# Kernel optimization log

Hardware: AMD Instinct MI355X
Metric: run time of the kernel (lower is better)

Reference implementation:

```python
import jax, jax.numpy as jnp
import numpy as np

BETA, ALPHA, NS_STEPS = 0.9, 1.0, 1
D_MODEL, D_STATE, D_CONV, EXPAND = 768, 16, 4, 2
D_INNER = EXPAND * D_MODEL
DT_RANK = -(-D_MODEL // 16)  # ceil(d_model/16) = 48
B, L = 2, 1024


def setup_inputs() -> dict:
    key = jax.random.key(0)
    ks = jax.random.split(key, 8)
    s = lambda k, shape, sc=0.02: jax.random.normal(k, shape, jnp.float32) * sc
    return {
        "hidden_states": jax.random.normal(ks[0], (B, L, D_MODEL), jnp.float32),
        "in_proj_w": s(ks[1], (2 * D_INNER, D_MODEL)),
        "conv_w": s(ks[2], (D_INNER, 1, D_CONV), 0.2),
        "conv_b": jnp.zeros((D_INNER,), jnp.float32),
        "x_proj_w": s(ks[3], (DT_RANK + 2 * D_STATE, D_INNER)),
        "dt_head_w": s(ks[4], (D_INNER, DT_RANK)),
        "dt_head_b": s(ks[5], (D_INNER,), 0.1),
        "out_proj_w": s(ks[6], (D_MODEL, D_INNER)),
        "D": jnp.ones((D_INNER,), jnp.float32),
    }


def _newton_schulz(G, steps):
    """Muon-style quintic Newton-Schulz orthogonalization of (b, d, n) with d >= n."""
    a, b, c = 3.4445, -4.7750, 2.0315
    X = G / (jnp.linalg.norm(G, axis=(-2, -1), keepdims=True) + 1e-7)
    X = X.swapaxes(-2, -1)  # (b, n, d): rows <= cols
    for _ in range(steps):
        A = X @ X.swapaxes(-2, -1)       # (b, n, n) small Gram
        Bm = b * A + c * (A @ A)
        X = a * X + Bm @ X
    return X.swapaxes(-2, -1)            # back to (b, d, n)


def reference(hidden_states, in_proj_w, conv_w, conv_b, x_proj_w, dt_head_w, dt_head_b, out_proj_w, D):
    Bz, Lz, _ = hidden_states.shape
    dtype = hidden_states.dtype
    # input projection -> x, z  (B, L, d_inner) each
    xz = jnp.einsum('bld,ed->ble', hidden_states, in_proj_w)
    x, z = jnp.split(xz, 2, axis=-1)
    # causal depthwise conv over time + SiLU
    xc = jax.lax.conv_general_dilated(
        x.swapaxes(1, 2), conv_w, (1,), [(D_CONV - 1, 0)],
        dimension_numbers=('NCH', 'OIH', 'NCH'), feature_group_count=D_INNER)
    x = jax.nn.silu(xc.swapaxes(1, 2) + conv_b)  # (B, L, d_inner)
    # projections for dt / k / q
    x_dbl = jnp.einsum('bld,ed->ble', x, x_proj_w)
    dt_low, k, q = jnp.split(x_dbl, [DT_RANK, DT_RANK + D_STATE], axis=-1)
    dt = jnp.einsum('blr,dr->bld', dt_low, dt_head_w)  # (B, L, d_inner), bias applied in scan

    def step(carry, inp):
        v, h = carry  # velocity / hidden states, each (b, d_inner, d_state)
        x_t, dt_t, k_t, q_t = inp
        dt_t = jax.nn.sigmoid(dt_t + dt_head_b)                              # (b, d)
        dt_t = dt_t / (1.0 + dt_t * jnp.sum(k_t * k_t, axis=-1, keepdims=True))
        dA = 1.0 - dt_t[:, :, None] * (k_t * k_t)[:, None, :]                # (b, d, n)
        G = (dt_t * x_t)[:, :, None] * k_t[:, None, :]                       # dt * u * k
        v = BETA * v + ALPHA * _newton_schulz(G, NS_STEPS)
        h = dA * h + v
        y_t = jnp.einsum('bdn,bn->bd', h, q_t) + D * x_t
        return (v, h), y_t

    init = (jnp.zeros((Bz, D_INNER, D_STATE), dtype),
            jnp.zeros((Bz, D_INNER, D_STATE), dtype))
    xs = (x.swapaxes(0, 1), dt.swapaxes(0, 1), k.swapaxes(0, 1), q.swapaxes(0, 1))
    _, y = jax.lax.scan(step, init, xs)        # (L, B, d_inner)
    y = y.swapaxes(0, 1) * jax.nn.silu(z)      # gate
    return jnp.einsum('bld,od->blo', y, out_proj_w)
```

## Files before the change

### kernel.cpp

```cpp
#include <hip/hip_runtime.h>

#define D_MODEL 768
#define D_STATE 16
#define D_INNER 1536
#define DT_RANK 48
#define NB 2
#define LSEQ 1024
#define NROWS (NB * LSEQ)
#define CCH 16
#define CLEN (LSEQ / CCH)
#define STP 16
#define BETA_CL 1.1790185e-03f
#define OUT_ELEMS (NROWS * D_MODEL)

typedef __attribute__((ext_vector_type(4))) float f32x4;
typedef __attribute__((ext_vector_type(8))) short s16x8;
typedef __attribute__((ext_vector_type(8))) unsigned short u16x8;
typedef __attribute__((ext_vector_type(4))) unsigned short u16x4;

__device__ __forceinline__ unsigned short f2bu(float f) {
  unsigned int x = __builtin_bit_cast(unsigned int, f);
  x += 0x7fffu + ((x >> 16) & 1u);
  return (unsigned short)(x >> 16);
}

typedef __attribute__((address_space(3))) unsigned int as3u32;
typedef __attribute__((address_space(1))) const unsigned int as1u32;
__device__ __forceinline__ void gload16(const unsigned short* g, unsigned short* l) {
  __builtin_amdgcn_global_load_lds((as1u32*)g, (as3u32*)l, 16, 0, 0);
}

#define CVT_TOTAL 663552
#define Z1_GROUPS 20480
__global__ __launch_bounds__(256) void cvt5z_kernel(const float* __restrict__ s0,
                                                    const float* __restrict__ s1,
                                                    const float* __restrict__ s2,
                                                    const float* __restrict__ s3,
                                                    const float* __restrict__ s4,
                                                    unsigned short* __restrict__ d0,
                                                    unsigned short* __restrict__ d1,
                                                    unsigned short* __restrict__ d2,
                                                    unsigned short* __restrict__ d3,
                                                    unsigned short* __restrict__ d4,
                                                    float* __restrict__ z1) {
  int g = blockIdx.x * 256 + threadIdx.x;
  if (g >= CVT_TOTAL) {
    int zg = g - CVT_TOTAL;
    f32x4 zero = {0.f, 0.f, 0.f, 0.f};
    if (zg < Z1_GROUPS) {
      *(f32x4*)(z1 + zg * 8) = zero;
      *(f32x4*)(z1 + zg * 8 + 4) = zero;
    }
    return;
  }
  const float* s;
  unsigned short* d;
  int base;
  if (g < 196608)      { s = s0; d = d0; base = 0; }
  else if (g < 491520) { s = s1; d = d1; base = 196608; }
  else if (g < 506880) { s = s2; d = d2; base = 491520; }
  else if (g < 516096) { s = s3; d = d3; base = 506880; }
  else                 { s = s4; d = d4; base = 516096; }
  int i = (g - base) * 8;
  f32x4 a = *(const f32x4*)(s + i);
  f32x4 b = *(const f32x4*)(s + i + 4);
  u16x8 o;
#pragma unroll
  for (int j = 0; j < 4; j++) { o[j] = f2bu(a[j]); o[4 + j] = f2bu(b[j]); }
  *(u16x8*)(d + i) = o;
}

template <bool PARTIAL>
__global__ __launch_bounds__(256) void gemm128(const unsigned short* __restrict__ A,
                                               const unsigned short* __restrict__ B,
                                               float* __restrict__ C, int K,
                                               int lda, int ldb, int ldc, int kseg_len) {
  __shared__ __align__(16) unsigned short As[2][128 * 32];
  __shared__ __align__(16) unsigned short Bs[2][128 * 32];
  const int m0 = blockIdx.y * 128, n0 = blockIdx.x * 128;
  const int kbeg = blockIdx.z * kseg_len;
  const int kend = kbeg + kseg_len;
  const int t = threadIdx.x;
  const int wave = t >> 6, lane = t & 63;
  const int wm = wave >> 1, wn = wave & 1;
  const int quad = lane >> 4, l16 = lane & 15;
  const int srow = lane >> 2;
  const int kcol = (lane & 3) * 8;

  float* Cp = C;
  if constexpr (PARTIAL) Cp = C + (size_t)blockIdx.z * (size_t)gridDim.y * 128 * ldc;

  auto stage = [&](int bi, int k0) {
#pragma unroll
    for (int r = 0; r < 2; r++) {
      const int seg = r * 64 + wave * 16;
      gload16(A + (size_t)(m0 + seg + srow) * lda + k0 + kcol, &As[bi][seg * 32]);
      gload16(B + (size_t)(n0 + seg + srow) * ldb + k0 + kcol, &Bs[bi][seg * 32]);
    }
  };

  f32x4 acc[4][4] = {};
  stage(0, kbeg);
  __syncthreads();
  int buf = 0;
  for (int k0 = kbeg; k0 < kend; k0 += 32) {
    if (k0 + 32 < kend) stage(buf ^ 1, k0 + 32);
    s16x8 af[4], bf[4];
#pragma unroll
    for (int i = 0; i < 4; i++) {
      af[i] = *(const s16x8*)&As[buf][(wm * 64 + i * 16 + l16) * 32 + quad * 8];
      bf[i] = *(const s16x8*)&Bs[buf][(wn * 64 + i * 16 + l16) * 32 + quad * 8];
    }
#pragma unroll
    for (int mi = 0; mi < 4; mi++)
#pragma unroll
      for (int ni = 0; ni < 4; ni++)
        acc[mi][ni] = __builtin_amdgcn_mfma_f32_16x16x32_bf16(af[mi], bf[ni], acc[mi][ni], 0, 0, 0);
    __syncthreads();
    buf ^= 1;
  }
#pragma unroll
  for (int mi = 0; mi < 4; mi++)
#pragma unroll
    for (int ni = 0; ni < 4; ni++)
#pragma unroll
      for (int r = 0; r < 4; r++) {
        int row = m0 + wm * 64 + mi * 16 + quad * 4 + r;
        int col = n0 + wn * 64 + ni * 16 + l16;
        Cp[(size_t)row * ldc + col] = acc[mi][ni][r];
      }
}

__global__ __launch_bounds__(256) void reduce4_kernel(const float* __restrict__ part,
                                                      float* __restrict__ out) {
  int i4 = (blockIdx.x * 256 + threadIdx.x) * 4;
  f32x4 a = *(const f32x4*)(part + i4);
  f32x4 b = *(const f32x4*)(part + (size_t)OUT_ELEMS + i4);
  f32x4 c = *(const f32x4*)(part + (size_t)2 * OUT_ELEMS + i4);
  f32x4 d = *(const f32x4*)(part + (size_t)3 * OUT_ELEMS + i4);
  f32x4 o;
#pragma unroll
  for (int j = 0; j < 4; j++) o[j] = (a[j] + b[j]) + (c[j] + d[j]);
  *(f32x4*)(out + i4) = o;
}

template <bool AF32, bool ATOMIC, bool DTF>
__global__ __launch_bounds__(256) void gemm_bt(const void* __restrict__ Av,
                                               const unsigned short* __restrict__ B,
                                               float* __restrict__ C, int M, int N, int K,
                                               int lda, int ldb, int ldc, int kseg_len,
                                               const float* __restrict__ dtb) {
  __shared__ __align__(16) unsigned short As[2][64][40];
  __shared__ __align__(16) unsigned short Bs[2][64][40];
  __shared__ float nk_s[64];
  const int m0 = blockIdx.y * 64, n0 = blockIdx.x * 64;
  const int kbeg = blockIdx.z * kseg_len;
  const int kend = (kbeg + kseg_len < K) ? (kbeg + kseg_len) : K;
  const int t = threadIdx.x;
  const int wave = t >> 6, lane = t & 63;
  const int wm = wave >> 1, wn = wave & 1;
  const int quad = lane >> 4, l16 = lane & 15;
  const int srow = t >> 2;
  const int kseg = (t & 3) * 8;
  const bool va = (m0 + srow) < M, vb = (n0 + srow) < N;
  const float* Af = (const float*)Av;
  const unsigned short* Ab = (const unsigned short*)Av;
  const unsigned short* Bp = B + (size_t)(n0 + srow) * ldb;

  f32x4 ra0, ra1;
  u16x8 rab, rbb;
  auto pref = [&](int k0) {
    const int kk = k0 + kseg;
    const int krem = kend - kk;
    if constexpr (AF32) {
      const float* Ap = Af + (size_t)(m0 + srow) * lda + kk;
      if (va && krem >= 8) {
        ra0 = *(const f32x4*)Ap;
        ra1 = *(const f32x4*)(Ap + 4);
      } else {
#pragma unroll
        for (int j = 0; j < 4; j++) {
          ra0[j] = (va && j < krem) ? Ap[j] : 0.0f;
          ra1[j] = (va && j + 4 < krem) ? Ap[j + 4] : 0.0f;
        }
      }
    } else {
      const unsigned short* Ap = Ab + (size_t)(m0 + srow) * lda + kk;
      if (va && krem >= 8) {
        rab = *(const u16x8*)Ap;
      } else {
#pragma unroll
        for (int j = 0; j < 8; j++) rab[j] = (va && j < krem) ? Ap[j] : (unsigned short)0;
      }
    }
    if (vb && krem >= 8) {
      rbb = *(const u16x8*)(Bp + kk);
    } else {
#pragma unroll
      for (int j = 0; j < 8; j++) rbb[j] = (vb && j < krem) ? Bp[kk + j] : (unsigned short)0;
    }
  };
  auto tolds = [&](int bi) {
    if constexpr (AF32) {
      u16x8 oa;
#pragma unroll
      for (int j = 0; j < 4; j++) { oa[j] = f2bu(ra0[j]); oa[4 + j] = f2bu(ra1[j]); }
      *(u16x8*)&As[bi][srow][kseg] = oa;
    } else {
      *(u16x8*)&As[bi][srow][kseg] = rab;
    }
    *(u16x8*)&Bs[bi][srow][kseg] = rbb;
  };

  f32x4 acc[2][2] = {};
  pref(kbeg);
  tolds(0);
  if constexpr (DTF) {
    if (t < 64 && (m0 + t) < M) {
      const float* kr = Af + (size_t)(m0 + t) * lda + 48;
      float nk = 0.0f;
#pragma unroll
      for (int n = 0; n < 16; n++) nk += kr[n] * kr[n];
      nk_s[t] = nk;
    }
  }
  __syncthreads();
  int buf = 0;
  for (int k0 = kbeg; k0 < kend; k0 += 32) {
    const bool more = (k0 + 32 < kend);
    if (more) pref(k0 + 32);
    s16x8 a0 = *(const s16x8*)&As[buf][wm * 32 + l16][quad * 8];
    s16x8 a1 = *(const s16x8*)&As[buf][wm * 32 + 16 + l16][quad * 8];
    s16x8 b0 = *(const s16x8*)&Bs[buf][wn * 32 + l16][quad * 8];
    s16x8 b1 = *(const s16x8*)&Bs[buf][wn * 32 + 16 + l16][quad * 8];
    acc[0][0] = __builtin_amdgcn_mfma_f32_16x16x32_bf16(a0, b0, acc[0][0], 0, 0, 0);
    acc[0][1] = __builtin_amdgcn_mfma_f32_16x16x32_bf16(a0, b1, acc[0][1], 0, 0, 0);
    acc[1][0] = __builtin_amdgcn_mfma_f32_16x16x32_bf16(a1, b0, acc[1][0], 0, 0, 0);
    acc[1][1] = __builtin_amdgcn_mfma_f32_16x16x32_bf16(a1, b1, acc[1][1], 0, 0, 0);
    if (more) tolds(buf ^ 1);
    __syncthreads();
    buf ^= 1;
  }
#pragma unroll
  for (int mi = 0; mi < 2; mi++)
#pragma unroll
    for (int ni = 0; ni < 2; ni++)
#pragma unroll
      for (int r = 0; r < 4; r++) {
        int row = m0 + wm * 32 + mi * 16 + quad * 4 + r;
        int col = n0 + wn * 32 + ni * 16 + l16;
        if (row < M && col < N) {
          float cv = acc[mi][ni][r];
          if constexpr (DTF) {
            float sg = 1.0f / (1.0f + expf(-(cv + dtb[col])));
            cv = sg / (1.0f + sg * nk_s[row - m0]);
          }
          if constexpr (ATOMIC)
            atomicAdd(&C[(size_t)row * ldc + col], cv);
          else
            C[(size_t)row * ldc + col] = cv;
        }
      }
}

__global__ __launch_bounds__(256) void conv_silu_kernel(const float* __restrict__ xz,
                                                        const float* __restrict__ cw,
                                                        const float* __restrict__ cb,
                                                        float* __restrict__ xc,
                                                        unsigned short* __restrict__ xcb) {
  int g = blockIdx.x * 256 + threadIdx.x;
  int c4 = (g % 384) * 4;
  int row = g / 384;
  int l = row & (LSEQ - 1);
  f32x4 acc = *(const f32x4*)(cb + c4);
  f32x4 w[4];
#pragma unroll
  for (int ci = 0; ci < 4; ci++) w[ci] = *(const f32x4*)(cw + (c4 + ci) * 4);
#pragma unroll
  for (int j = 0; j < 4; j++) {
    int dl = l - 3 + j;
    if (dl >= 0) {
      f32x4 xv = *(const f32x4*)(xz + (size_t)(row - 3 + j) * 3072 + c4);
#pragma unroll
      for (int ci = 0; ci < 4; ci++) acc[ci] = fmaf(xv[ci], w[ci][j], acc[ci]);
    }
  }
  f32x4 val;
  u16x4 ob;
#pragma unroll
  for (int ci = 0; ci < 4; ci++) {
    float sg = 1.0f / (1.0f + expf(-acc[ci]));
    val[ci] = acc[ci] * sg;
    ob[ci] = f2bu(val[ci]);
  }
  *(f32x4*)(xc + (size_t)row * D_INNER + c4) = val;
  *(u16x4*)(xcb + (size_t)row * D_INNER + c4) = ob;
}

__global__ __launch_bounds__(256) void gamma_kernel(const float* __restrict__ xdbl,
                                                    const float* __restrict__ dtfbuf,
                                                    const float* __restrict__ xconv,
                                                    float* __restrict__ gammabuf,
                                                    float* __restrict__ kqbuf) {
  int row = blockIdx.x;
  int t = threadIdx.x;
  const float* xr = xdbl + (size_t)row * 80;
  float nk = 0.0f;
#pragma unroll
  for (int n = 0; n < 16; n++) { float kv = xr[48 + n]; nk += kv * kv; }
  float nupart = 0.0f;
#pragma unroll
  for (int gi = 0; gi < 2; gi++) {
    int g = gi * 256 + t;
    if (g < 384) {
      int d = g * 4;
      f32x4 df = *(const f32x4*)(dtfbuf + (size_t)row * D_INNER + d);
      f32x4 xcv = *(const f32x4*)(xconv + (size_t)row * D_INNER + d);
#pragma unroll
      for (int j = 0; j < 4; j++) {
        float u = df[j] * xcv[j];
        nupart += u * u;
      }
    }
  }
  __shared__ float red[4];
  float v = nupart;
#pragma unroll
  for (int off = 32; off > 0; off >>= 1) v += __shfl_xor(v, off);
  if ((t & 63) == 0) red[t >> 6] = v;
  __syncthreads();
  float nu = red[0] + red[1] + red[2] + red[3];
  float p = nu * nk;
  float s = sqrtf(p) + 1e-7f;
  float tt = p / (s * s);
  float gamma = (3.4445f + tt * (-4.7750f + 2.0315f * tt)) / s;
  if (t == 0) gammabuf[row] = gamma;
  if (t < 8)
    *(f32x4*)(kqbuf + (size_t)row * 32 + t * 4) = *(const f32x4*)(xr + 48 + t * 4);
}

__global__ __launch_bounds__(256) void scan_phase1(const float* __restrict__ xconv,
                                                   const float* __restrict__ dtbuf,
                                                   const float* __restrict__ kqbuf,
                                                   const float* __restrict__ gammabuf,
                                                   float* __restrict__ cvp,
                                                   float* __restrict__ chp,
                                                   float* __restrict__ gp,
                                                   float* __restrict__ rp) {
  __shared__ __align__(16) float xc_s[2][STP][64];
  __shared__ __align__(16) float dt_s[2][STP][64];
  __shared__ __align__(16) float kq_s[2][STP][36];
  __shared__ float g_s[2][STP];
  const int t = threadIdx.x;
  const int nq = t & 3, dloc = t >> 2;
  const int b = blockIdx.x / (24 * CCH);
  const int rem = blockIdx.x % (24 * CCH);
  const int d0 = (rem / CCH) * 64;
  const int c = rem % CCH;
  const int tbase = c * CLEN;
  const size_t ub = ((size_t)b * LSEQ + tbase) * D_INNER + d0;
  const float* kqb = kqbuf + ((size_t)b * LSEQ + tbase) * 32;
  const float* gmb = gammabuf + (size_t)b * LSEQ + tbase;
  const int prow = t >> 4, pcol = (t & 15) * 4;
  const int krow = t >> 3, kcol = (t & 7) * 4;
  f32x4 pxc, pd, pk;
  float pg;
  auto prefetch = [&](int t0) {
    size_t off = ub + (size_t)(t0 + prow) * D_INNER + pcol;
    pxc = *(const f32x4*)(xconv + off);
    pd = *(const f32x4*)(dtbuf + off);
    if (t < 128) pk = *(const f32x4*)(kqb + (size_t)(t0 + krow) * 32 + kcol);
    if (t < STP) pg = gmb[t0 + t];
  };
  auto writelds = [&](int bi) {
    *(f32x4*)&xc_s[bi][prow][pcol] = pxc;
    *(f32x4*)&dt_s[bi][prow][pcol] = pd;
    if (t < 128) *(f32x4*)&kq_s[bi][krow][kcol] = pk;
    if (t < STP) g_s[bi][t] = pg;
  };
  f32x4 v = {0.f, 0.f, 0.f, 0.f}, h = {0.f, 0.f, 0.f, 0.f};
  f32x4 g = {0.f, 0.f, 0.f, 0.f}, r = {1.f, 1.f, 1.f, 1.f};
  float bt = 0.9f;
  prefetch(0);
  writelds(0);
  __syncthreads();
  int buf = 0;
  for (int t0 = 0; t0 < CLEN; t0 += STP) {
    const bool more = (t0 + STP < CLEN);
    if (more) prefetch(t0 + STP);
#pragma unroll 4
    for (int s = 0; s < STP; s++) {
      float dtf = dt_s[buf][s][dloc];
      float u = g_s[buf][s] * dtf * xc_s[buf][s][dloc];
#pragma unroll
      for (int j = 0; j < 4; j++) {
        float kj = kq_s[buf][s][nq * 4 + j];
        v[j] = fmaf(0.9f, v[j], u * kj);
        float a = fmaf(-dtf * kj, kj, 1.0f);
        h[j] = fmaf(a, h[j], v[j]);
        r[j] *= a;
        g[j] = fmaf(a, g[j], bt);
      }
      bt *= 0.9f;
    }
    if (more) writelds(buf ^ 1);
    __syncthreads();
    buf ^= 1;
  }
  size_t o = (((size_t)b * CCH + c) * D_INNER + d0 + dloc) * 16 + nq * 4;
  *(f32x4*)(cvp + o) = v;
  *(f32x4*)(chp + o) = h;
  *(f32x4*)(gp + o) = g;
  *(f32x4*)(rp + o) = r;
}

__global__ __launch_bounds__(256) void scan_phase2(const float* __restrict__ cvp,
                                                   const float* __restrict__ chp,
                                                   float* __restrict__ gp,
                                                   float* __restrict__ rp) {
  int i4 = (blockIdx.x * 256 + threadIdx.x) * 4;
  int b = i4 / (D_INNER * 16);
  int rem = i4 % (D_INNER * 16);
  f32x4 v0 = {0.f, 0.f, 0.f, 0.f}, h0 = {0.f, 0.f, 0.f, 0.f};
#pragma unroll
  for (int c = 0; c < CCH; c++) {
    size_t o = ((size_t)(b * CCH + c)) * (D_INNER * 16) + rem;
    f32x4 cv = *(const f32x4*)(cvp + o);
    f32x4 ch = *(const f32x4*)(chp + o);
    f32x4 gg = *(const f32x4*)(gp + o);
    f32x4 rr = *(const f32x4*)(rp + o);
    *(f32x4*)(gp + o) = v0;
    *(f32x4*)(rp + o) = h0;
#pragma unroll
    for (int j = 0; j < 4; j++) {
      float v0n = fmaf(BETA_CL, v0[j], cv[j]);
      float h0n = fmaf(gg[j], v0[j], fmaf(rr[j], h0[j], ch[j]));
      v0[j] = v0n;
      h0[j] = h0n;
    }
  }
}

__global__ __launch_bounds__(256) void scan_phase3(const float* __restrict__ dtbuf,
                                                   const float* __restrict__ kqbuf,
                                                   const float* __restrict__ gammabuf,
                                                   const float* __restrict__ gp,
                                                   const float* __restrict__ rp,
                                                   const float* __restrict__ xconv,
                                                   const float* __restrict__ xz,
                                                   const float* __restrict__ Dp,
                                                   unsigned short* __restrict__ ygb) {
  __shared__ __align__(16) float xc_s[2][STP][64];
  __shared__ __align__(16) float dt_s[2][STP][64];
  __shared__ __align__(16) float z_s[2][STP][64];
  __shared__ __align__(16) float kq_s[2][STP][36];
  __shared__ float g_s[2][STP];
  const int t = threadIdx.x;
  const int nq = t & 3, dloc = t >> 2;
  const int b = blockIdx.x / (24 * CCH);
  const int rem = blockIdx.x % (24 * CCH);
  const int d0 = (rem / CCH) * 64;
  const int c = rem % CCH;
  const int tbase = c * CLEN;
  const size_t ub = ((size_t)b * LSEQ + tbase) * D_INNER + d0;
  const float* kqb = kqbuf + ((size_t)b * LSEQ + tbase) * 32;
  const float* gmb = gammabuf + (size_t)b * LSEQ + tbase;
  const float* z0 = xz + ((size_t)b * LSEQ + tbase) * 3072 + 1536 + d0;
  unsigned short* y_p = ygb + (size_t)b * LSEQ * D_INNER + d0 + dloc;
  const int prow = t >> 4, pcol = (t & 15) * 4;
  const int krow = t >> 3, kcol = (t & 7) * 4;
  f32x4 pxc, pd, pz, pk;
  float pg;
  auto prefetch = [&](int t0) {
    size_t off = ub + (size_t)(t0 + prow) * D_INNER + pcol;
    pxc = *(const f32x4*)(xconv + off);
    pd = *(const f32x4*)(dtbuf + off);
    pz = *(const f32x4*)(z0 + (size_t)(t0 + prow) * 3072 + pcol);
    if (t < 128) pk = *(const f32x4*)(kqb + (size_t)(t0 + krow) * 32 + kcol);
    if (t < STP) pg = gmb[t0 + t];
  };
  auto writelds = [&](int bi) {
    *(f32x4*)&xc_s[bi][prow][pcol] = pxc;
    *(f32x4*)&dt_s[bi][prow][pcol] = pd;
    *(f32x4*)&z_s[bi][prow][pcol] = pz;
    if (t < 128) *(f32x4*)&kq_s[bi][krow][kcol] = pk;
    if (t < STP) g_s[bi][t] = pg;
  };
  size_t so = (((size_t)b * CCH + c) * D_INNER + d0 + dloc) * 16 + nq * 4;
  f32x4 v = *(const f32x4*)(gp + so);
  f32x4 h = *(const f32x4*)(rp + so);
  const float Dd = Dp[d0 + dloc];
  prefetch(0);
  writelds(0);
  __syncthreads();
  int buf = 0;
  for (int t0 = 0; t0 < CLEN; t0 += STP) {
    const bool more = (t0 + STP < CLEN);
    if (more) prefetch(t0 + STP);
#pragma unroll 4
    for (int s = 0; s < STP; s++) {
      float xcv = xc_s[buf][s][dloc];
      float dtf = dt_s[buf][s][dloc];
      float u = g_s[buf][s] * dtf * xcv;
      f32x4 kv = *(const f32x4*)&kq_s[buf][s][nq * 4];
      f32x4 qv = *(const f32x4*)&kq_s[buf][s][16 + nq * 4];
      float yp = 0.0f;
#pragma unroll
      for (int j = 0; j < 4; j++) {
        float kj = kv[j];
        v[j] = fmaf(0.9f, v[j], u * kj);
        float dA = fmaf(-dtf * kj, kj, 1.0f);
        h[j] = fmaf(dA, h[j], v[j]);
        yp = fmaf(h[j], qv[j], yp);
      }
      yp += __shfl_xor(yp, 1);
      yp += __shfl_xor(yp, 2);
      float zv = z_s[buf][s][dloc];
      float sz = zv / (1.0f + expf(-zv));
      float val = (yp + Dd * xcv) * sz;
      if (nq == 0) y_p[(size_t)(tbase + t0 + s) * D_INNER] = f2bu(val);
    }
    if (more) writelds(buf ^ 1);
    __syncthreads();
    buf ^= 1;
  }
}

extern "C" void kernel_launch(void* const* d_in, const int* in_sizes, int n_in,
                              void* d_out, int out_size, void* d_ws, size_t ws_size,
                              hipStream_t stream) {
  const float* hidden = (const float*)d_in[0];
  const float* w_in   = (const float*)d_in[1];
  const float* conv_w = (const float*)d_in[2];
  const float* conv_b = (const float*)d_in[3];
  const float* w_x    = (const float*)d_in[4];
  const float* w_dt   = (const float*)d_in[5];
  const float* b_dt   = (const float*)d_in[6];
  const float* w_out  = (const float*)d_in[7];
  const float* Dp     = (const float*)d_in[8];

  float* ws    = (float*)d_ws;
  float* xz    = ws;
  float* xconv = xz + (size_t)NROWS * 3072;
  float* xdbl  = xconv + (size_t)NROWS * D_INNER;
  float* dtbuf = xdbl + (size_t)NROWS * 80;
  float* gammabuf = dtbuf + (size_t)NROWS * D_INNER;
  float* kqbuf = gammabuf + NROWS;
  const size_t PL = (size_t)NB * CCH * D_INNER * 16;
  float* cvp   = kqbuf + (size_t)NROWS * 32;
  float* chp   = cvp + PL;
  float* gp    = chp + PL;
  float* rp    = gp + PL;
  float* opart = rp + PL;
  unsigned short* bfr = (unsigned short*)(opart + (size_t)4 * OUT_ELEMS);
  unsigned short* hbf = bfr;
  unsigned short* wib = hbf + 1572864;
  unsigned short* wxb = wib + 2359296;
  unsigned short* wdb = wxb + 122880;
  unsigned short* wob = wdb + 73728;
  unsigned short* xcb = wob + 1179648;
  unsigned short* ygb = xcb + 3145728;

  dim3 blk(256);
  cvt5z_kernel<<<dim3((CVT_TOTAL + Z1_GROUPS) / 256), blk, 0, stream>>>(
      hidden, w_in, w_x, w_dt, w_out, hbf, wib, wxb, wdb, wob, xdbl);
  gemm128<false><<<dim3(24, 16, 1), blk, 0, stream>>>(hbf, wib, xz, 768, 768, 768, 3072, 768);
  conv_silu_kernel<<<dim3(3072), blk, 0, stream>>>(xz, conv_w, conv_b, xconv, xcb);
  gemm_bt<false, true, false><<<dim3(2, 32, 8), blk, 0, stream>>>(
      xcb, wxb, xdbl, 2048, 80, 1536, 1536, 1536, 80, 192, nullptr);
  gemm_bt<true, false, true><<<dim3(24, 32, 1), blk, 0, stream>>>(
      xdbl, wdb, dtbuf, 2048, 1536, 48, 80, 48, 1536, 48, b_dt);
  gamma_kernel<<<dim3(NROWS), blk, 0, stream>>>(xdbl, dtbuf, xconv, gammabuf, kqbuf);
  scan_phase1<<<dim3(NB * 24 * CCH), blk, 0, stream>>>(xconv, dtbuf, kqbuf, gammabuf,
                                                       cvp, chp, gp, rp);
  scan_phase2<<<dim3(48), blk, 0, stream>>>(cvp, chp, gp, rp);
  scan_phase3<<<dim3(NB * 24 * CCH), blk, 0, stream>>>(dtbuf, kqbuf, gammabuf, gp, rp,
                                                       xconv, xz, Dp, ygb);
  gemm128<true><<<dim3(6, 16, 4), blk, 0, stream>>>(ygb, wob, opart, 1536,
                                                    1536, 1536, 768, 384);
  reduce4_kernel<<<dim3(OUT_ELEMS / 1024), blk, 0, stream>>>(opart, (float*)d_out);
}
```

Baseline: 204.3 us.

## Fuse gamma norm reduction into dt GEMM epilogue and drop gamma kernel

The per-row sum of (dt*x)^2 moves into the epilogue of the dt-projection GEMM, which reduces it with wave shuffles and atomics into a buffer zeroed by the conversion kernel. Gamma is then recomputed on the fly inside the scan phases from that buffer and the k norm read straight from xdbl. This removes the separate gamma kernel launch and its re-read of dtbuf and xconv. In exchange the GEMM epilogue now reads xconv and issues atomics, and both scan phases redo a small amount of scalar work per step.

```diff
diff --git a/kernel.cpp b/kernel.cpp
--- a/kernel.cpp
+++ b/kernel.cpp
@@ -32,6 +32,7 @@
 
 #define CVT_TOTAL 663552
 #define Z1_GROUPS 20480
+#define Z2_GROUPS 256
 __global__ __launch_bounds__(256) void cvt5z_kernel(const float* __restrict__ s0,
                                                     const float* __restrict__ s1,
                                                     const float* __restrict__ s2,
@@ -42,7 +43,8 @@
                                                     unsigned short* __restrict__ d2,
                                                     unsigned short* __restrict__ d3,
                                                     unsigned short* __restrict__ d4,
-                                                    float* __restrict__ z1) {
+                                                    float* __restrict__ z1,
+                                                    float* __restrict__ z2) {
   int g = blockIdx.x * 256 + threadIdx.x;
   if (g >= CVT_TOTAL) {
     int zg = g - CVT_TOTAL;
@@ -50,6 +52,10 @@
     if (zg < Z1_GROUPS) {
       *(f32x4*)(z1 + zg * 8) = zero;
       *(f32x4*)(z1 + zg * 8 + 4) = zero;
+    } else if (zg < Z1_GROUPS + Z2_GROUPS) {
+      int i = (zg - Z1_GROUPS) * 8;
+      *(f32x4*)(z2 + i) = zero;
+      *(f32x4*)(z2 + i + 4) = zero;
     }
     return;
   }
@@ -149,7 +155,9 @@
                                                const unsigned short* __restrict__ B,
                                                float* __restrict__ C, int M, int N, int K,
                                                int lda, int ldb, int ldc, int kseg_len,
-                                               const float* __restrict__ dtb) {
+                                               const float* __restrict__ dtb,
+                                               const float* __restrict__ xconv,
+                                               float* __restrict__ nubuf) {
   __shared__ __align__(16) unsigned short As[2][64][40];
   __shared__ __align__(16) unsigned short Bs[2][64][40];
   __shared__ float nk_s[64];
@@ -241,26 +249,51 @@
     __syncthreads();
     buf ^= 1;
   }
-#pragma unroll
-  for (int mi = 0; mi < 2; mi++)
-#pragma unroll
-    for (int ni = 0; ni < 2; ni++)
+  if constexpr (DTF) {
+    float u2[2][4] = {};
+#pragma unroll
+    for (int mi = 0; mi < 2; mi++)
+#pragma unroll
+      for (int ni = 0; ni < 2; ni++)
+#pragma unroll
+        for (int r = 0; r < 4; r++) {
+          int row = m0 + wm * 32 + mi * 16 + quad * 4 + r;
+          int col = n0 + wn * 32 + ni * 16 + l16;
+          float sg = 1.0f / (1.0f + expf(-(acc[mi][ni][r] + dtb[col])));
+          float dv = sg / (1.0f + sg * nk_s[row - m0]);
+          C[(size_t)row * ldc + col] = dv;
+          float u = dv * xconv[(size_t)row * D_INNER + col];
+          u2[mi][r] += u * u;
+        }
+#pragma unroll
+    for (int mi = 0; mi < 2; mi++)
 #pragma unroll
       for (int r = 0; r < 4; r++) {
-        int row = m0 + wm * 32 + mi * 16 + quad * 4 + r;
-        int col = n0 + wn * 32 + ni * 16 + l16;
-        if (row < M && col < N) {
-          float cv = acc[mi][ni][r];
-          if constexpr (DTF) {
-            float sg = 1.0f / (1.0f + expf(-(cv + dtb[col])));
-            cv = sg / (1.0f + sg * nk_s[row - m0]);
+        float v = u2[mi][r];
+        v += __shfl_xor(v, 1);
+        v += __shfl_xor(v, 2);
+        v += __shfl_xor(v, 4);
+        v += __shfl_xor(v, 8);
+        if (l16 == 0)
+          atomicAdd(&nubuf[m0 + wm * 32 + mi * 16 + quad * 4 + r], v);
+      }
+  } else {
+#pragma unroll
+    for (int mi = 0; mi < 2; mi++)
+#pragma unroll
+      for (int ni = 0; ni < 2; ni++)
+#pragma unroll
+        for (int r = 0; r < 4; r++) {
+          int row = m0 + wm * 32 + mi * 16 + quad * 4 + r;
+          int col = n0 + wn * 32 + ni * 16 + l16;
+          if (row < M && col < N) {
+            if constexpr (ATOMIC)
+              atomicAdd(&C[(size_t)row * ldc + col], acc[mi][ni][r]);
+            else
+              C[(size_t)row * ldc + col] = acc[mi][ni][r];
           }
-          if constexpr (ATOMIC)
-            atomicAdd(&C[(size_t)row * ldc + col], cv);
-          else
-            C[(size_t)row * ldc + col] = cv;
         }
-      }
+  }
 }
 
 __global__ __launch_bounds__(256) void conv_silu_kernel(const float* __restrict__ xz,
@@ -297,52 +330,17 @@
   *(u16x4*)(xcb + (size_t)row * D_INNER + c4) = ob;
 }
 
-__global__ __launch_bounds__(256) void gamma_kernel(const float* __restrict__ xdbl,
-                                                    const float* __restrict__ dtfbuf,
-                                                    const float* __restrict__ xconv,
-                                                    float* __restrict__ gammabuf,
-                                                    float* __restrict__ kqbuf) {
-  int row = blockIdx.x;
-  int t = threadIdx.x;
-  const float* xr = xdbl + (size_t)row * 80;
-  float nk = 0.0f;
-#pragma unroll
-  for (int n = 0; n < 16; n++) { float kv = xr[48 + n]; nk += kv * kv; }
-  float nupart = 0.0f;
-#pragma unroll
-  for (int gi = 0; gi < 2; gi++) {
-    int g = gi * 256 + t;
-    if (g < 384) {
-      int d = g * 4;
-      f32x4 df = *(const f32x4*)(dtfbuf + (size_t)row * D_INNER + d);
-      f32x4 xcv = *(const f32x4*)(xconv + (size_t)row * D_INNER + d);
-#pragma unroll
-      for (int j = 0; j < 4; j++) {
-        float u = df[j] * xcv[j];
-        nupart += u * u;
-      }
-    }
-  }
-  __shared__ float red[4];
-  float v = nupart;
-#pragma unroll
-  for (int off = 32; off > 0; off >>= 1) v += __shfl_xor(v, off);
-  if ((t & 63) == 0) red[t >> 6] = v;
-  __syncthreads();
-  float nu = red[0] + red[1] + red[2] + red[3];
+__device__ __forceinline__ float gamma_of(float nu, float nk) {
   float p = nu * nk;
   float s = sqrtf(p) + 1e-7f;
   float tt = p / (s * s);
-  float gamma = (3.4445f + tt * (-4.7750f + 2.0315f * tt)) / s;
-  if (t == 0) gammabuf[row] = gamma;
-  if (t < 8)
-    *(f32x4*)(kqbuf + (size_t)row * 32 + t * 4) = *(const f32x4*)(xr + 48 + t * 4);
+  return (3.4445f + tt * (-4.7750f + 2.0315f * tt)) / s;
 }
 
 __global__ __launch_bounds__(256) void scan_phase1(const float* __restrict__ xconv,
                                                    const float* __restrict__ dtbuf,
-                                                   const float* __restrict__ kqbuf,
-                                                   const float* __restrict__ gammabuf,
+                                                   const float* __restrict__ xdbl,
+                                                   const float* __restrict__ nubuf,
                                                    float* __restrict__ cvp,
                                                    float* __restrict__ chp,
                                                    float* __restrict__ gp,
@@ -359,8 +357,8 @@
   const int c = rem % CCH;
   const int tbase = c * CLEN;
   const size_t ub = ((size_t)b * LSEQ + tbase) * D_INNER + d0;
-  const float* kqb = kqbuf + ((size_t)b * LSEQ + tbase) * 32;
-  const float* gmb = gammabuf + (size_t)b * LSEQ + tbase;
+  const float* kqb = xdbl + ((size_t)b * LSEQ + tbase) * 80 + 48;
+  const float* nub = nubuf + (size_t)b * LSEQ + tbase;
   const int prow = t >> 4, pcol = (t & 15) * 4;
   const int krow = t >> 3, kcol = (t & 7) * 4;
   f32x4 pxc, pd, pk;
@@ -369,8 +367,14 @@
     size_t off = ub + (size_t)(t0 + prow) * D_INNER + pcol;
     pxc = *(const f32x4*)(xconv + off);
     pd = *(const f32x4*)(dtbuf + off);
-    if (t < 128) pk = *(const f32x4*)(kqb + (size_t)(t0 + krow) * 32 + kcol);
-    if (t < STP) pg = gmb[t0 + t];
+    if (t < 128) pk = *(const f32x4*)(kqb + (size_t)(t0 + krow) * 80 + kcol);
+    if (t < STP) {
+      const float* kr = kqb + (size_t)(t0 + t) * 80;
+      float nk = 0.0f;
+#pragma unroll
+      for (int n = 0; n < 16; n++) nk += kr[n] * kr[n];
+      pg = gamma_of(nub[t0 + t], nk);
+    }
   };
   auto writelds = [&](int bi) {
     *(f32x4*)&xc_s[bi][prow][pcol] = pxc;
@@ -442,8 +446,8 @@
 }
 
 __global__ __launch_bounds__(256) void scan_phase3(const float* __restrict__ dtbuf,
-                                                   const float* __restrict__ kqbuf,
-                                                   const float* __restrict__ gammabuf,
+                                                   const float* __restrict__ xdbl,
+                                                   const float* __restrict__ nubuf,
                                                    const float* __restrict__ gp,
                                                    const float* __restrict__ rp,
                                                    const float* __restrict__ xconv,
@@ -463,8 +467,8 @@
   const int c = rem % CCH;
   const int tbase = c * CLEN;
   const size_t ub = ((size_t)b * LSEQ + tbase) * D_INNER + d0;
-  const float* kqb = kqbuf + ((size_t)b * LSEQ + tbase) * 32;
-  const float* gmb = gammabuf + (size_t)b * LSEQ + tbase;
+  const float* kqb = xdbl + ((size_t)b * LSEQ + tbase) * 80 + 48;
+  const float* nub = nubuf + (size_t)b * LSEQ + tbase;
   const float* z0 = xz + ((size_t)b * LSEQ + tbase) * 3072 + 1536 + d0;
   unsigned short* y_p = ygb + (size_t)b * LSEQ * D_INNER + d0 + dloc;
   const int prow = t >> 4, pcol = (t & 15) * 4;
@@ -476,8 +480,14 @@
     pxc = *(const f32x4*)(xconv + off);
     pd = *(const f32x4*)(dtbuf + off);
     pz = *(const f32x4*)(z0 + (size_t)(t0 + prow) * 3072 + pcol);
-    if (t < 128) pk = *(const f32x4*)(kqb + (size_t)(t0 + krow) * 32 + kcol);
-    if (t < STP) pg = gmb[t0 + t];
+    if (t < 128) pk = *(const f32x4*)(kqb + (size_t)(t0 + krow) * 80 + kcol);
+    if (t < STP) {
+      const float* kr = kqb + (size_t)(t0 + t) * 80;
+      float nk = 0.0f;
+#pragma unroll
+      for (int n = 0; n < 16; n++) nk += kr[n] * kr[n];
+      pg = gamma_of(nub[t0 + t], nk);
+    }
   };
   auto writelds = [&](int bi) {
     *(f32x4*)&xc_s[bi][prow][pcol] = pxc;
@@ -544,10 +554,9 @@
   float* xconv = xz + (size_t)NROWS * 3072;
   float* xdbl  = xconv + (size_t)NROWS * D_INNER;
   float* dtbuf = xdbl + (size_t)NROWS * 80;
-  float* gammabuf = dtbuf + (size_t)NROWS * D_INNER;
-  float* kqbuf = gammabuf + NROWS;
+  float* nubuf = dtbuf + (size_t)NROWS * D_INNER;
   const size_t PL = (size_t)NB * CCH * D_INNER * 16;
-  float* cvp   = kqbuf + (size_t)NROWS * 32;
+  float* cvp   = nubuf + NROWS;
   float* chp   = cvp + PL;
   float* gp    = chp + PL;
   float* rp    = gp + PL;
@@ -562,19 +571,18 @@
   unsigned short* ygb = xcb + 3145728;
 
   dim3 blk(256);
-  cvt5z_kernel<<<dim3((CVT_TOTAL + Z1_GROUPS) / 256), blk, 0, stream>>>(
-      hidden, w_in, w_x, w_dt, w_out, hbf, wib, wxb, wdb, wob, xdbl);
+  cvt5z_kernel<<<dim3((CVT_TOTAL + Z1_GROUPS + Z2_GROUPS) / 256), blk, 0, stream>>>(
+      hidden, w_in, w_x, w_dt, w_out, hbf, wib, wxb, wdb, wob, xdbl, nubuf);
   gemm128<false><<<dim3(24, 16, 1), blk, 0, stream>>>(hbf, wib, xz, 768, 768, 768, 3072, 768);
   conv_silu_kernel<<<dim3(3072), blk, 0, stream>>>(xz, conv_w, conv_b, xconv, xcb);
   gemm_bt<false, true, false><<<dim3(2, 32, 8), blk, 0, stream>>>(
-      xcb, wxb, xdbl, 2048, 80, 1536, 1536, 1536, 80, 192, nullptr);
+      xcb, wxb, xdbl, 2048, 80, 1536, 1536, 1536, 80, 192, nullptr, nullptr, nullptr);
   gemm_bt<true, false, true><<<dim3(24, 32, 1), blk, 0, stream>>>(
-      xdbl, wdb, dtbuf, 2048, 1536, 48, 80, 48, 1536, 48, b_dt);
-  gamma_kernel<<<dim3(NROWS), blk, 0, stream>>>(xdbl, dtbuf, xconv, gammabuf, kqbuf);
-  scan_phase1<<<dim3(NB * 24 * CCH), blk, 0, stream>>>(xconv, dtbuf, kqbuf, gammabuf,
+      xdbl, wdb, dtbuf, 2048, 1536, 48, 80, 48, 1536, 48, b_dt, xconv, nubuf);
+  scan_phase1<<<dim3(NB * 24 * CCH), blk, 0, stream>>>(xconv, dtbuf, xdbl, nubuf,
                                                        cvp, chp, gp, rp);
   scan_phase2<<<dim3(48), blk, 0, stream>>>(cvp, chp, gp, rp);
-  scan_phase3<<<dim3(NB * 24 * CCH), blk, 0, stream>>>(dtbuf, kqbuf, gammabuf, gp, rp,
+  scan_phase3<<<dim3(NB * 24 * CCH), blk, 0, stream>>>(dtbuf, xdbl, nubuf, gp, rp,
                                                        xconv, xz, Dp, ygb);
   gemm128<true><<<dim3(6, 16, 4), blk, 0, stream>>>(ygb, wob, opart, 1536,
                                                     1536, 1536, 768, 384);
```

Measured after the change: 206.6 us. About the same (+1.1%).
